# Kernel tuning notes

Measured on AMD Instinct MI355X. Metric: run time of the kernel, lower is better.

Reference implementation:

```python
import jax, jax.numpy as jnp
import numpy as np

EPS = 1e-6

def rmsnorm(x, w):
    return x * jax.lax.rsqrt(jnp.mean(x * x, axis=-1, keepdims=True) + EPS) * w

def hard_sigmoid(x):
    # relu6(x + 3) / 6 - 0.5
    return jnp.clip(x + 3.0, 0.0, 6.0) / 6.0 - 0.5

def setup_inputs() -> dict:
    key = jax.random.key(0)
    ks = jax.random.split(key, 8)
    B, T, C, E = 4, 4096, 1024, 4
    H = E * C
    x = jax.random.normal(ks[0], (B, T, C), dtype=jnp.float32)
    norm1_w = jnp.ones((C,), dtype=jnp.float32)
    norm2_w = jnp.ones((C,), dtype=jnp.float32)
    s1 = 1.0 / np.sqrt(C)
    s2 = 1.0 / np.sqrt(H)
    mlp1_w = jax.random.uniform(ks[1], (C, C), jnp.float32, -s1, s1)
    mlp1_b = jax.random.uniform(ks[2], (C,), jnp.float32, -s1, s1)
    mlp2a_w = jax.random.uniform(ks[3], (C, H), jnp.float32, -s1, s1)
    mlp2a_b = jax.random.uniform(ks[4], (H,), jnp.float32, -s1, s1)
    mlp2b_w = jax.random.uniform(ks[5], (H, C), jnp.float32, -s2, s2)
    mlp2b_b = jax.random.uniform(ks[6], (C,), jnp.float32, -s2, s2)
    return {"x": x, "norm1_w": norm1_w, "mlp1_w": mlp1_w, "mlp1_b": mlp1_b,
            "norm2_w": norm2_w, "mlp2a_w": mlp2a_w, "mlp2a_b": mlp2a_b,
            "mlp2b_w": mlp2b_w, "mlp2b_b": mlp2b_b}

def reference(x, norm1_w, mlp1_w, mlp1_b, norm2_w, mlp2a_w, mlp2a_b, mlp2b_w, mlp2b_b):
    # state: [B, T, C] prefix sum over time of gated, normalized input
    state = jnp.cumsum(hard_sigmoid(rmsnorm(x, norm1_w)), axis=1)
    out = hard_sigmoid(state @ mlp1_w + mlp1_b) * x
    h = jax.nn.relu(rmsnorm(out, norm2_w) @ mlp2a_w + mlp2a_b)
    return h @ mlp2b_w + mlp2b_b + out
```

## Files before the change

### kernel.cpp

```cpp
#include <hip/hip_runtime.h>

#define B_     4
#define T_     4096
#define C_     1024
#define H_     4096
#define BT_    (B_ * T_)
#define NCH_   64
#define CHLEN_ 64
#define MCHUNK 8192

typedef __bf16 bf16_t;
typedef __bf16 bf16x8 __attribute__((ext_vector_type(8)));
typedef float  f32x4  __attribute__((ext_vector_type(4)));

__device__ __forceinline__ float hs_f(float v) {
    return fminf(fmaxf((v + 3.0f) * (1.0f / 6.0f), 0.0f), 1.0f) - 0.5f;
}

__device__ __forceinline__ void gld_lds16(const bf16_t* g, bf16_t* l) {
    __builtin_amdgcn_global_load_lds((const __attribute__((address_space(1))) void*)g,
                                     (__attribute__((address_space(3))) void*)l,
                                     16, 0, 0);
}

__global__ __launch_bounds__(256) void rms_rows_f32(const float* __restrict__ X,
                                                    float* __restrict__ inv) {
    const int wave = threadIdx.x >> 6, lane = threadIdx.x & 63;
    const int row = blockIdx.x * 4 + wave;
    const float* xr = X + (size_t)row * C_;
    float s = 0.0f;
    #pragma unroll
    for (int p = 0; p < 4; p++) {
        float4 v = *(const float4*)(xr + p * 256 + lane * 4);
        s += v.x * v.x + v.y * v.y + v.z * v.z + v.w * v.w;
    }
    #pragma unroll
    for (int o = 32; o > 0; o >>= 1) s += __shfl_down(s, o, 64);
    if (lane == 0) inv[row] = rsqrtf(s * (1.0f / C_) + 1e-6f);
}

__global__ __launch_bounds__(256) void scan_emit_local(const float* __restrict__ X,
                                                       const float* __restrict__ inv1,
                                                       const float* __restrict__ nw,
                                                       bf16_t* __restrict__ state,
                                                       float* __restrict__ csum) {
    const int bch = blockIdx.x;
    const int b = bch >> 6, ch = bch & 63;
    const int c = blockIdx.y * 256 + threadIdx.x;
    const float wgt = nw[c];
    const int rbase = b * T_ + ch * CHLEN_;
    const size_t xbase = (size_t)rbase * C_ + c;
    float acc = 0.0f;
    for (int i = 0; i < CHLEN_; i++) {
        acc += hs_f(X[xbase + (size_t)i * C_] * inv1[rbase + i] * wgt);
        state[(size_t)(rbase + i) * C_ + c] = (bf16_t)acc;
    }
    csum[(size_t)bch * C_ + c] = acc;
}

__global__ __launch_bounds__(256) void scan_offsets_hilo(const float* __restrict__ csum,
                                                         bf16_t* __restrict__ hilo) {
    const int idx = blockIdx.x * 256 + threadIdx.x;
    const int b = idx >> 10, c = idx & 1023;
    const size_t base = (size_t)b * NCH_ * C_ + c;
    float v[NCH_];
    #pragma unroll
    for (int ch = 0; ch < NCH_; ch++)
        v[ch] = csum[base + (size_t)ch * C_];
    float run = 0.0f;
    #pragma unroll
    for (int ch = 0; ch < NCH_; ch++) {
        const size_t row = (size_t)(b * NCH_ + ch) * 2048 + c;
        const bf16_t hi = (bf16_t)run;
        hilo[row] = hi;
        hilo[row + 1024] = (bf16_t)(run - (float)hi);
        run += v[ch];
    }
}

__global__ __launch_bounds__(256) void pmat_init(const float* __restrict__ b1,
                                                 float* __restrict__ Pmat,
                                                 float* __restrict__ rs2) {
    const int i = blockIdx.x * 256 + threadIdx.x;
    Pmat[i] = b1[i & (C_ - 1)];
    if (i < BT_) rs2[i] = 0.0f;
}

__global__ __launch_bounds__(256) void inv_finish(const float* __restrict__ rs2,
                                                  float* __restrict__ inv) {
    const int i = blockIdx.x * 256 + threadIdx.x;
    inv[i] = rsqrtf(rs2[i] * (1.0f / C_) + 1e-6f);
}

__global__ __launch_bounds__(256) void transpose_all(const float* __restrict__ w1,
                                                     const float* __restrict__ w2a,
                                                     const float* __restrict__ w2b,
                                                     const float* __restrict__ n2w,
                                                     bf16_t* __restrict__ W1cat,
                                                     bf16_t* __restrict__ W2at,
                                                     bf16_t* __restrict__ W2bt) {
    __shared__ float tile[32][33];
    const int flat = blockIdx.x;
    const float* src; bf16_t* dst; const float* scale;
    int N, ldd, dupOff, bx, by;
    if (flat < 1024) {
        src = w1; dst = W1cat; scale = nullptr;
        N = C_; ldd = 2048; dupOff = 1024;
        bx = flat & 31; by = flat >> 5;
    } else if (flat < 5120) {
        const int f = flat - 1024;
        src = w2a; dst = W2at; scale = n2w;
        N = H_; ldd = C_; dupOff = 0;
        bx = f & 127; by = f >> 7;
    } else {
        const int f = flat - 5120;
        src = w2b; dst = W2bt; scale = nullptr;
        N = C_; ldd = H_; dupOff = 0;
        bx = f & 31; by = f >> 5;
    }
    const int n0 = bx * 32, k0 = by * 32;
    const int tx = threadIdx.x & 31, ty = threadIdx.x >> 5;
    #pragma unroll
    for (int j = 0; j < 4; j++) {
        const int kk = ty + j * 8;
        float v = src[(size_t)(k0 + kk) * N + n0 + tx];
        if (scale) v *= scale[k0 + kk];
        tile[kk][tx] = v;
    }
    __syncthreads();
    #pragma unroll
    for (int j = 0; j < 4; j++) {
        const int nn = ty + j * 8;
        const bf16_t v = (bf16_t)tile[tx][nn];
        dst[(size_t)(n0 + nn) * ldd + k0 + tx] = v;
        if (dupOff) dst[(size_t)(n0 + nn) * ldd + dupOff + k0 + tx] = v;
    }
}

template <int MODE, typename ET, typename OT>
__global__ __launch_bounds__(256) void gemm_bt(const bf16_t* __restrict__ A,
                                               const bf16_t* __restrict__ Bt,
                                               const float* __restrict__ bias,
                                               const ET* __restrict__ extra,
                                               const float* __restrict__ rowscale,
                                               const float* __restrict__ pmat,
                                               float* __restrict__ aux,
                                               OT* __restrict__ Cmat,
                                               int N, int K, int lda, int ldb) {
    __shared__ __align__(16) bf16_t As[2][128 * 32];
    __shared__ __align__(16) bf16_t Bs[2][128 * 32];
    const int tid = threadIdx.x;

    const int nwgx = gridDim.x;
    const int flat0 = blockIdx.y * nwgx + blockIdx.x;
    int mTile, nTile;
    if ((nwgx & 7) == 0) {
        const int xcd = flat0 & 7;
        const int loc = flat0 >> 3;
        const int mpx = nwgx >> 3;
        mTile = xcd * mpx + (loc % mpx);
        nTile = loc / mpx;
    } else {
        mTile = blockIdx.x;
        nTile = blockIdx.y;
    }
    const int mBase = mTile * 128;
    const int nBase = nTile * 128;
    const size_t kOff = (size_t)blockIdx.z * K;

    const int wave = tid >> 6;
    const int lane = tid & 63;
    const int waveM = (wave & 1) * 64;
    const int waveN = (wave >> 1) * 64;
    const int lr = lane & 15;
    const int lq = lane >> 4;

    f32x4 acc[4][4] = {};

    const int e0 = tid * 8;
    const int r0 = e0 >> 5, c0 = (((e0 >> 3) & 3) ^ ((r0 >> 1) & 3)) << 3;
    const int e1 = 2048 + tid * 8;
    const int r1 = e1 >> 5, c1 = (((e1 >> 3) & 3) ^ ((r1 >> 1) & 3)) << 3;

    const bf16_t* Ag0 = A + (size_t)(mBase + r0) * lda + kOff + c0;
    const bf16_t* Ag1 = A + (size_t)(mBase + r1) * lda + kOff + c1;
    const bf16_t* Bg0 = Bt + (size_t)(nBase + r0) * ldb + kOff + c0;
    const bf16_t* Bg1 = Bt + (size_t)(nBase + r1) * ldb + kOff + c1;

    auto stage = [&](int buf, int kb) {
        gld_lds16(Ag0 + kb, As[buf] + e0);
        gld_lds16(Ag1 + kb, As[buf] + e1);
        gld_lds16(Bg0 + kb, Bs[buf] + e0);
        gld_lds16(Bg1 + kb, Bs[buf] + e1);
    };

    stage(0, 0);
    if (32 < K) stage(1, 32);

    int cur = 0;
    for (int kb = 0; kb < K; kb += 32) {
        if (kb + 32 < K) asm volatile("s_waitcnt vmcnt(4)" ::: "memory");
        else             asm volatile("s_waitcnt vmcnt(0)" ::: "memory");
        __builtin_amdgcn_s_barrier();

        bf16x8 af[4], bfr[4];
        #pragma unroll
        for (int mi = 0; mi < 4; mi++) {
            const int R = waveM + mi * 16 + lr;
            af[mi] = *(const bf16x8*)(As[cur] + R * 32 + ((lq ^ ((R >> 1) & 3)) << 3));
        }
        #pragma unroll
        for (int ni = 0; ni < 4; ni++) {
            const int R = waveN + ni * 16 + lr;
            bfr[ni] = *(const bf16x8*)(Bs[cur] + R * 32 + ((lq ^ ((R >> 1) & 3)) << 3));
        }
        #pragma unroll
        for (int mi = 0; mi < 4; mi++)
            #pragma unroll
            for (int ni = 0; ni < 4; ni++)
                acc[mi][ni] = __builtin_amdgcn_mfma_f32_16x16x32_bf16(
                    af[mi], bfr[ni], acc[mi][ni], 0, 0, 0);

        __builtin_amdgcn_s_barrier();
        if (kb + 64 < K) stage(cur, kb + 64);
        cur ^= 1;
    }

    float sq[4][4];
    if (MODE == 0) {
        #pragma unroll
        for (int a = 0; a < 4; a++)
            #pragma unroll
            for (int b = 0; b < 4; b++) sq[a][b] = 0.0f;
    }
    #pragma unroll
    for (int ni = 0; ni < 4; ni++) {
        const int n = nBase + waveN + ni * 16 + lr;
        const float bz = (MODE == 1 || MODE == 2) ? bias[n] : 0.0f;
        #pragma unroll
        for (int mi = 0; mi < 4; mi++) {
            #pragma unroll
            for (int r = 0; r < 4; r++) {
                const int m = mBase + waveM + mi * 16 + lq * 4 + r;
                float v = acc[mi][ni][r];
                if (MODE == 0) {
                    v = hs_f(v + pmat[(size_t)(m >> 6) * N + n]) * (float)extra[(size_t)m * N + n];
                    const OT vs = (OT)v;
                    Cmat[(size_t)m * N + n] = vs;
                    const float vb = (float)vs;
                    sq[mi][r] += vb * vb;
                } else if (MODE == 1) {
                    v = fmaxf(rowscale[m] * v + bz, 0.0f);
                    Cmat[(size_t)m * N + n] = (OT)v;
                } else if (MODE == 2) {
                    v = v + bz + (float)extra[(size_t)m * N + n];
                    Cmat[(size_t)m * N + n] = (OT)v;
                } else {
                    atomicAdd((float*)&Cmat[(size_t)m * N + n], v);
                }
            }
        }
    }
    if (MODE == 0) {
        #pragma unroll
        for (int mi = 0; mi < 4; mi++) {
            #pragma unroll
            for (int r = 0; r < 4; r++) {
                float s = sq[mi][r];
                s += __shfl_xor(s, 1, 64);
                s += __shfl_xor(s, 2, 64);
                s += __shfl_xor(s, 4, 64);
                s += __shfl_xor(s, 8, 64);
                if (lr == 0) {
                    const int m = mBase + waveM + mi * 16 + lq * 4 + r;
                    atomicAdd(&aux[m], s);
                }
            }
        }
    }
}

extern "C" void kernel_launch(void* const* d_in, const int* in_sizes, int n_in,
                              void* d_out, int out_size, void* d_ws, size_t ws_size,
                              hipStream_t stream) {
    const float* x   = (const float*)d_in[0];
    const float* n1w = (const float*)d_in[1];
    const float* w1  = (const float*)d_in[2];
    const float* b1  = (const float*)d_in[3];
    const float* n2w = (const float*)d_in[4];
    const float* w2a = (const float*)d_in[5];
    const float* b2a = (const float*)d_in[6];
    const float* w2b = (const float*)d_in[7];
    const float* b2b = (const float*)d_in[8];
    float* y = (float*)d_out;

    char* w = (char*)d_ws;
    float*  inv1  = (float*)(w + 0);
    float*  inv2  = (float*)(w + 65536);
    float*  csum  = (float*)(w + 131072);
    bf16_t* hilo  = (bf16_t*)(w + 1179648);
    float*  Pmat  = (float*)(w + 2228224);
    bf16_t* W1cat = (bf16_t*)(w + 5373952);
    bf16_t* W2at  = (bf16_t*)(w + 9568256);
    bf16_t* W2bt  = (bf16_t*)(w + 17956864);
    bf16_t* outb  = (bf16_t*)(w + 26345472);
    bf16_t* state = (bf16_t*)(w + 59899904);
    bf16_t* hbuf  = state;
    float*  rs2   = csum;

    rms_rows_f32<<<dim3(BT_ / 4), dim3(256), 0, stream>>>(x, inv1);
    scan_emit_local<<<dim3(B_ * NCH_, C_ / 256), dim3(256), 0, stream>>>(x, inv1, n1w, state, csum);
    scan_offsets_hilo<<<dim3(B_ * C_ / 256), dim3(256), 0, stream>>>(csum, hilo);
    transpose_all<<<dim3(9216), dim3(256), 0, stream>>>(
        w1, w2a, w2b, n2w, W1cat, W2at, W2bt);
    pmat_init<<<dim3(256 * C_ / 256), dim3(256), 0, stream>>>(b1, Pmat, rs2);
    gemm_bt<4, float, float><<<dim3(2, C_ / 128, 4), dim3(256), 0, stream>>>(
        hilo, W1cat, nullptr, nullptr, nullptr, nullptr, nullptr, Pmat, C_, 512, 2048, 2048);
    gemm_bt<0, float, bf16_t><<<dim3(BT_ / 128, C_ / 128), dim3(256), 0, stream>>>(
        state, W1cat, nullptr, x, nullptr, Pmat, rs2, outb, C_, C_, C_, 2048);
    inv_finish<<<dim3(BT_ / 256), dim3(256), 0, stream>>>(rs2, inv2);
    for (int c = 0; c < BT_ / MCHUNK; c++) {
        const bf16_t* Ao = outb + (size_t)c * MCHUNK * C_;
        float* yo = y + (size_t)c * MCHUNK * C_;
        gemm_bt<1, float, bf16_t><<<dim3(MCHUNK / 128, H_ / 128), dim3(256), 0, stream>>>(
            Ao, W2at, b2a, nullptr, inv2 + c * MCHUNK, nullptr, nullptr, hbuf, H_, C_, C_, C_);
        gemm_bt<2, bf16_t, float><<<dim3(MCHUNK / 128, C_ / 128), dim3(256), 0, stream>>>(
            hbuf, W2bt, b2b, Ao, nullptr, nullptr, nullptr, yo, C_, H_, H_, H_);
    }
}
```

Before: 605.7 us.

## Enlarge GEMM tiles to 256x128 with 8 waves and fold small kernels

```diff
diff --git a/kernel.cpp b/kernel.cpp
--- a/kernel.cpp
+++ b/kernel.cpp
@@ -78,29 +78,24 @@
     }
 }
 
-__global__ __launch_bounds__(256) void pmat_init(const float* __restrict__ b1,
-                                                 float* __restrict__ Pmat,
-                                                 float* __restrict__ rs2) {
-    const int i = blockIdx.x * 256 + threadIdx.x;
-    Pmat[i] = b1[i & (C_ - 1)];
-    if (i < BT_) rs2[i] = 0.0f;
-}
-
-__global__ __launch_bounds__(256) void inv_finish(const float* __restrict__ rs2,
-                                                  float* __restrict__ inv) {
-    const int i = blockIdx.x * 256 + threadIdx.x;
-    inv[i] = rsqrtf(rs2[i] * (1.0f / C_) + 1e-6f);
-}
-
 __global__ __launch_bounds__(256) void transpose_all(const float* __restrict__ w1,
                                                      const float* __restrict__ w2a,
                                                      const float* __restrict__ w2b,
                                                      const float* __restrict__ n2w,
+                                                     const float* __restrict__ b1,
                                                      bf16_t* __restrict__ W1cat,
                                                      bf16_t* __restrict__ W2at,
-                                                     bf16_t* __restrict__ W2bt) {
+                                                     bf16_t* __restrict__ W2bt,
+                                                     float* __restrict__ Pmat,
+                                                     float* __restrict__ rs2) {
+    const int flat = blockIdx.x;
+    if (flat >= 9216) {
+        const int i = (flat - 9216) * 256 + threadIdx.x;
+        Pmat[i] = b1[i & (C_ - 1)];
+        if (i < BT_) rs2[i] = 0.0f;
+        return;
+    }
     __shared__ float tile[32][33];
-    const int flat = blockIdx.x;
     const float* src; bf16_t* dst; const float* scale;
     int N, ldd, dupOff, bx, by;
     if (flat < 1024) {
@@ -137,8 +132,91 @@
     }
 }
 
+__global__ __launch_bounds__(256) void gemm_pk(const bf16_t* __restrict__ A,
+                                               const bf16_t* __restrict__ Bt,
+                                               float* __restrict__ Cmat,
+                                               int N, int K, int lda, int ldb) {
+    __shared__ __align__(16) bf16_t As[2][128 * 32];
+    __shared__ __align__(16) bf16_t Bs[2][128 * 32];
+    const int tid = threadIdx.x;
+    const int mBase = blockIdx.x * 128;
+    const int nBase = blockIdx.y * 128;
+    const size_t kOff = (size_t)blockIdx.z * K;
+
+    const int wave = tid >> 6;
+    const int lane = tid & 63;
+    const int waveM = (wave & 1) * 64;
+    const int waveN = (wave >> 1) * 64;
+    const int lr = lane & 15;
+    const int lq = lane >> 4;
+
+    f32x4 acc[4][4] = {};
+
+    const int e0 = tid * 8;
+    const int r0 = e0 >> 5, c0 = (((e0 >> 3) & 3) ^ ((r0 >> 1) & 3)) << 3;
+    const int e1 = 2048 + tid * 8;
+    const int r1 = e1 >> 5, c1 = (((e1 >> 3) & 3) ^ ((r1 >> 1) & 3)) << 3;
+
+    const bf16_t* Ag0 = A + (size_t)(mBase + r0) * lda + kOff + c0;
+    const bf16_t* Ag1 = A + (size_t)(mBase + r1) * lda + kOff + c1;
+    const bf16_t* Bg0 = Bt + (size_t)(nBase + r0) * ldb + kOff + c0;
+    const bf16_t* Bg1 = Bt + (size_t)(nBase + r1) * ldb + kOff + c1;
+
+    auto stage = [&](int buf, int kb) {
+        gld_lds16(Ag0 + kb, As[buf] + e0);
+        gld_lds16(Ag1 + kb, As[buf] + e1);
+        gld_lds16(Bg0 + kb, Bs[buf] + e0);
+        gld_lds16(Bg1 + kb, Bs[buf] + e1);
+    };
+
+    stage(0, 0);
+    if (32 < K) stage(1, 32);
+
+    int cur = 0;
+    for (int kb = 0; kb < K; kb += 32) {
+        if (kb + 32 < K) asm volatile("s_waitcnt vmcnt(4)" ::: "memory");
+        else             asm volatile("s_waitcnt vmcnt(0)" ::: "memory");
+        __builtin_amdgcn_s_barrier();
+
+        bf16x8 af[4], bfr[4];
+        #pragma unroll
+        for (int mi = 0; mi < 4; mi++) {
+            const int R = waveM + mi * 16 + lr;
+            af[mi] = *(const bf16x8*)(As[cur] + R * 32 + ((lq ^ ((R >> 1) & 3)) << 3));
+        }
+        #pragma unroll
+        for (int ni = 0; ni < 4; ni++) {
+            const int R = waveN + ni * 16 + lr;
+            bfr[ni] = *(const bf16x8*)(Bs[cur] + R * 32 + ((lq ^ ((R >> 1) & 3)) << 3));
+        }
+        #pragma unroll
+        for (int mi = 0; mi < 4; mi++)
+            #pragma unroll
+            for (int ni = 0; ni < 4; ni++)
+                acc[mi][ni] = __builtin_amdgcn_mfma_f32_16x16x32_bf16(
+                    af[mi], bfr[ni], acc[mi][ni], 0, 0, 0);
+
+        __builtin_amdgcn_s_barrier();
+        if (kb + 64 < K) stage(cur, kb + 64);
+        cur ^= 1;
+    }
+
+    #pragma unroll
+    for (int ni = 0; ni < 4; ni++) {
+        const int n = nBase + waveN + ni * 16 + lr;
+        #pragma unroll
+        for (int mi = 0; mi < 4; mi++) {
+            #pragma unroll
+            for (int r = 0; r < 4; r++) {
+                const int m = mBase + waveM + mi * 16 + lq * 4 + r;
+                atomicAdd(&Cmat[(size_t)m * N + n], acc[mi][ni][r]);
+            }
+        }
+    }
+}
+
 template <int MODE, typename ET, typename OT>
-__global__ __launch_bounds__(256) void gemm_bt(const bf16_t* __restrict__ A,
+__global__ __launch_bounds__(512) void gemm_bt(const bf16_t* __restrict__ A,
                                                const bf16_t* __restrict__ Bt,
                                                const float* __restrict__ bias,
                                                const ET* __restrict__ extra,
@@ -147,7 +225,7 @@
                                                float* __restrict__ aux,
                                                OT* __restrict__ Cmat,
                                                int N, int K, int lda, int ldb) {
-    __shared__ __align__(16) bf16_t As[2][128 * 32];
+    __shared__ __align__(16) bf16_t As[2][256 * 32];
     __shared__ __align__(16) bf16_t Bs[2][128 * 32];
     const int tid = threadIdx.x;
 
@@ -164,34 +242,33 @@
         mTile = blockIdx.x;
         nTile = blockIdx.y;
     }
-    const int mBase = mTile * 128;
+    const int mBase = mTile * 256;
     const int nBase = nTile * 128;
-    const size_t kOff = (size_t)blockIdx.z * K;
 
     const int wave = tid >> 6;
     const int lane = tid & 63;
-    const int waveM = (wave & 1) * 64;
-    const int waveN = (wave >> 1) * 64;
+    const int waveM = (wave >> 1) * 64;
+    const int waveN = (wave & 1) * 64;
     const int lr = lane & 15;
     const int lq = lane >> 4;
 
     f32x4 acc[4][4] = {};
 
-    const int e0 = tid * 8;
-    const int r0 = e0 >> 5, c0 = (((e0 >> 3) & 3) ^ ((r0 >> 1) & 3)) << 3;
-    const int e1 = 2048 + tid * 8;
-    const int r1 = e1 >> 5, c1 = (((e1 >> 3) & 3) ^ ((r1 >> 1) & 3)) << 3;
-
-    const bf16_t* Ag0 = A + (size_t)(mBase + r0) * lda + kOff + c0;
-    const bf16_t* Ag1 = A + (size_t)(mBase + r1) * lda + kOff + c1;
-    const bf16_t* Bg0 = Bt + (size_t)(nBase + r0) * ldb + kOff + c0;
-    const bf16_t* Bg1 = Bt + (size_t)(nBase + r1) * ldb + kOff + c1;
+    const int a0 = tid * 8;
+    const int ar0 = a0 >> 5, ac0 = (((a0 >> 3) & 3) ^ ((ar0 >> 1) & 3)) << 3;
+    const int a1 = 4096 + tid * 8;
+    const int ar1 = a1 >> 5, ac1 = (((a1 >> 3) & 3) ^ ((ar1 >> 1) & 3)) << 3;
+    const int b0 = tid * 8;
+    const int br0 = b0 >> 5, bc0 = (((b0 >> 3) & 3) ^ ((br0 >> 1) & 3)) << 3;
+
+    const bf16_t* Ag0 = A + (size_t)(mBase + ar0) * lda + ac0;
+    const bf16_t* Ag1 = A + (size_t)(mBase + ar1) * lda + ac1;
+    const bf16_t* Bg0 = Bt + (size_t)(nBase + br0) * ldb + bc0;
 
     auto stage = [&](int buf, int kb) {
-        gld_lds16(Ag0 + kb, As[buf] + e0);
-        gld_lds16(Ag1 + kb, As[buf] + e1);
-        gld_lds16(Bg0 + kb, Bs[buf] + e0);
-        gld_lds16(Bg1 + kb, Bs[buf] + e1);
+        gld_lds16(Ag0 + kb, As[buf] + a0);
+        gld_lds16(Ag1 + kb, As[buf] + a1);
+        gld_lds16(Bg0 + kb, Bs[buf] + b0);
     };
 
     stage(0, 0);
@@ -199,7 +276,7 @@
 
     int cur = 0;
     for (int kb = 0; kb < K; kb += 32) {
-        if (kb + 32 < K) asm volatile("s_waitcnt vmcnt(4)" ::: "memory");
+        if (kb + 32 < K) asm volatile("s_waitcnt vmcnt(3)" ::: "memory");
         else             asm volatile("s_waitcnt vmcnt(0)" ::: "memory");
         __builtin_amdgcn_s_barrier();
 
@@ -227,11 +304,21 @@
     }
 
     float sq[4][4];
+    float invm[4][4];
     if (MODE == 0) {
         #pragma unroll
         for (int a = 0; a < 4; a++)
             #pragma unroll
             for (int b = 0; b < 4; b++) sq[a][b] = 0.0f;
+    }
+    if (MODE == 1) {
+        #pragma unroll
+        for (int mi = 0; mi < 4; mi++)
+            #pragma unroll
+            for (int r = 0; r < 4; r++) {
+                const int m = mBase + waveM + mi * 16 + lq * 4 + r;
+                invm[mi][r] = rsqrtf(rowscale[m] * (1.0f / C_) + 1e-6f);
+            }
     }
     #pragma unroll
     for (int ni = 0; ni < 4; ni++) {
@@ -250,13 +337,11 @@
                     const float vb = (float)vs;
                     sq[mi][r] += vb * vb;
                 } else if (MODE == 1) {
-                    v = fmaxf(rowscale[m] * v + bz, 0.0f);
+                    v = fmaxf(invm[mi][r] * v + bz, 0.0f);
                     Cmat[(size_t)m * N + n] = (OT)v;
-                } else if (MODE == 2) {
+                } else {
                     v = v + bz + (float)extra[(size_t)m * N + n];
                     Cmat[(size_t)m * N + n] = (OT)v;
-                } else {
-                    atomicAdd((float*)&Cmat[(size_t)m * N + n], v);
                 }
             }
         }
@@ -296,7 +381,6 @@
 
     char* w = (char*)d_ws;
     float*  inv1  = (float*)(w + 0);
-    float*  inv2  = (float*)(w + 65536);
     float*  csum  = (float*)(w + 131072);
     bf16_t* hilo  = (bf16_t*)(w + 1179648);
     float*  Pmat  = (float*)(w + 2228224);
@@ -311,20 +395,18 @@
     rms_rows_f32<<<dim3(BT_ / 4), dim3(256), 0, stream>>>(x, inv1);
     scan_emit_local<<<dim3(B_ * NCH_, C_ / 256), dim3(256), 0, stream>>>(x, inv1, n1w, state, csum);
     scan_offsets_hilo<<<dim3(B_ * C_ / 256), dim3(256), 0, stream>>>(csum, hilo);
-    transpose_all<<<dim3(9216), dim3(256), 0, stream>>>(
-        w1, w2a, w2b, n2w, W1cat, W2at, W2bt);
-    pmat_init<<<dim3(256 * C_ / 256), dim3(256), 0, stream>>>(b1, Pmat, rs2);
-    gemm_bt<4, float, float><<<dim3(2, C_ / 128, 4), dim3(256), 0, stream>>>(
-        hilo, W1cat, nullptr, nullptr, nullptr, nullptr, nullptr, Pmat, C_, 512, 2048, 2048);
-    gemm_bt<0, float, bf16_t><<<dim3(BT_ / 128, C_ / 128), dim3(256), 0, stream>>>(
+    transpose_all<<<dim3(10240), dim3(256), 0, stream>>>(
+        w1, w2a, w2b, n2w, b1, W1cat, W2at, W2bt, Pmat, rs2);
+    gemm_pk<<<dim3(2, C_ / 128, 4), dim3(256), 0, stream>>>(
+        hilo, W1cat, Pmat, C_, 512, 2048, 2048);
+    gemm_bt<0, float, bf16_t><<<dim3(BT_ / 256, C_ / 128), dim3(512), 0, stream>>>(
         state, W1cat, nullptr, x, nullptr, Pmat, rs2, outb, C_, C_, C_, 2048);
-    inv_finish<<<dim3(BT_ / 256), dim3(256), 0, stream>>>(rs2, inv2);
     for (int c = 0; c < BT_ / MCHUNK; c++) {
         const bf16_t* Ao = outb + (size_t)c * MCHUNK * C_;
         float* yo = y + (size_t)c * MCHUNK * C_;
-        gemm_bt<1, float, bf16_t><<<dim3(MCHUNK / 128, H_ / 128), dim3(256), 0, stream>>>(
-            Ao, W2at, b2a, nullptr, inv2 + c * MCHUNK, nullptr, nullptr, hbuf, H_, C_, C_, C_);
-        gemm_bt<2, bf16_t, float><<<dim3(MCHUNK / 128, C_ / 128), dim3(256), 0, stream>>>(
+        gemm_bt<1, float, bf16_t><<<dim3(MCHUNK / 256, H_ / 128), dim3(512), 0, stream>>>(
+            Ao, W2at, b2a, nullptr, rs2 + c * MCHUNK, nullptr, nullptr, hbuf, H_, C_, C_, C_);
+        gemm_bt<2, bf16_t, float><<<dim3(MCHUNK / 256, C_ / 128), dim3(512), 0, stream>>>(
             hbuf, W2bt, b2b, Ao, nullptr, nullptr, nullptr, yo, C_, H_, H_, H_);
     }
 }
```

After: 614.9 us. About the same (+1.5%).
